# Optimization experiments

Hardware: AMD Instinct MI355X
Metric: run time of the kernel (lower is better)

## Reference

```python
import jax, jax.numpy as jnp
import numpy as np

B, H, W, C = 16, 64, 64, 192
NH, WS, SHIFT = 6, 8, 4          # heads, window size, shift (window//2)
DEPTH, MLP_R = 2, 4
N = WS * WS                      # tokens per window = 64
HD = C // NH                     # head dim = 32
SCALE = HD ** -0.5
TBL = (2 * WS - 1) ** 2          # relative-bias table size = 225
NW = (H // WS) * (W // WS)       # windows per image = 64


def _rel_pos_index():
    coords = np.stack(np.meshgrid(np.arange(WS), np.arange(WS), indexing='ij')).reshape(2, -1)
    rel = (coords[:, :, None] - coords[:, None, :]).transpose(1, 2, 0)
    rel[..., 0] += WS - 1
    rel[..., 1] += WS - 1
    rel[..., 0] *= 2 * WS - 1
    return jnp.asarray(rel.sum(-1))  # [N, N] int


def _attn_mask():
    # Swin shifted-window mask: region ids then pairwise -100 where ids differ.
    img = np.zeros((H, W))
    sl = (slice(0, -WS), slice(-WS, -SHIFT), slice(-SHIFT, None))
    cnt = 0
    for hs in sl:
        for ws in sl:
            img[hs, ws] = cnt
            cnt += 1
    mw = img.reshape(H // WS, WS, W // WS, WS).transpose(0, 2, 1, 3).reshape(-1, N)
    diff = mw[:, None, :] - mw[:, :, None]
    return jnp.asarray(np.where(diff != 0, -100.0, 0.0).astype(np.float32))  # [NW, N, N]


REL_IDX = _rel_pos_index()
ATTN_MASK = _attn_mask()


def _ln(x, g, b, eps=1e-5):
    mu = x.mean(-1, keepdims=True)
    var = ((x - mu) ** 2).mean(-1, keepdims=True)
    return (x - mu) * jax.lax.rsqrt(var + eps) * g + b


def setup_inputs() -> dict:
    key = jax.random.key(0)
    ks = jax.random.split(key, 8)
    s = 0.02
    return {
        'x': jax.random.normal(ks[0], (B, H * W, C), jnp.float32),
        'norm1_g': jnp.ones((DEPTH, C)), 'norm1_b': jnp.zeros((DEPTH, C)),
        'qkv_w': jax.random.normal(ks[1], (DEPTH, 3 * C, C)) * s,
        'qkv_b': jnp.zeros((DEPTH, 3 * C)),
        'bias_table': jax.random.normal(ks[2], (DEPTH, TBL, NH)) * s,
        'proj_w': jax.random.normal(ks[3], (DEPTH, C, C)) * s,
        'proj_b': jnp.zeros((DEPTH, C)),
        'norm2_g': jnp.ones((DEPTH, C)), 'norm2_b': jnp.zeros((DEPTH, C)),
        'fc1_w': jax.random.normal(ks[4], (DEPTH, MLP_R * C, C)) * s,
        'fc1_b': jnp.zeros((DEPTH, MLP_R * C)),
        'fc2_w': jax.random.normal(ks[5], (DEPTH, C, MLP_R * C)) * s,
        'fc2_b': jnp.zeros((DEPTH, C)),
    }


def _block(x, shift, n1g, n1b, qw, qb, tbl, pw, pb, n2g, n2b, f1w, f1b, f2w, f2b):
    shortcut = x
    y = _ln(x, n1g, n1b).reshape(B, H, W, C)
    if shift > 0:
        y = jnp.roll(y, (-shift, -shift), axis=(1, 2))
    # window partition -> [B*NW, N, C]
    win = y.reshape(B, H // WS, WS, W // WS, WS, C).transpose(0, 1, 3, 2, 4, 5).reshape(-1, N, C)
    qkv = (win @ qw.T + qb).reshape(-1, N, 3, NH, HD).transpose(2, 0, 3, 1, 4)
    q, k, v = qkv[0] * SCALE, qkv[1], qkv[2]          # each [B*NW, NH, N, HD]
    attn = jnp.einsum('bhnd,bhmd->bhnm', q, k)
    attn = attn + tbl[REL_IDX].transpose(2, 0, 1)[None]  # relative position bias
    if shift > 0:
        attn = (attn.reshape(B, NW, NH, N, N) + ATTN_MASK[None, :, None]).reshape(-1, NH, N, N)
    attn = jax.nn.softmax(attn, axis=-1)
    o = jnp.einsum('bhnm,bhmd->bhnd', attn, v).transpose(0, 2, 1, 3).reshape(-1, N, C)
    o = o @ pw.T + pb
    # window reverse
    y = o.reshape(B, H // WS, W // WS, WS, WS, C).transpose(0, 1, 3, 2, 4, 5).reshape(B, H, W, C)
    if shift > 0:
        y = jnp.roll(y, (shift, shift), axis=(1, 2))
    x = shortcut + y.reshape(B, H * W, C)
    h = _ln(x, n2g, n2b)
    h = jax.nn.gelu(h @ f1w.T + f1b, approximate=False)  # torch nn.GELU = exact erf
    return x + (h @ f2w.T + f2b)


def reference(x, norm1_g, norm1_b, qkv_w, qkv_b, bias_table, proj_w, proj_b,
              norm2_g, norm2_b, fc1_w, fc1_b, fc2_w, fc2_b):
    for i in range(DEPTH):
        shift = 0 if i % 2 == 0 else SHIFT
        x = _block(x, shift, norm1_g[i], norm1_b[i], qkv_w[i], qkv_b[i], bias_table[i],
                   proj_w[i], proj_b[i], norm2_g[i], norm2_b[i],
                   fc1_w[i], fc1_b[i], fc2_w[i], fc2_b[i])
    return x
```

## Files before the change

### kernel.cpp

```cpp
#include <hip/hip_runtime.h>
#include <hip/hip_bf16.h>
#include <math.h>

typedef __hip_bfloat16 bf16;
typedef short bf16x8 __attribute__((ext_vector_type(8)));
typedef short s16x4 __attribute__((ext_vector_type(4)));
typedef float f32x4 __attribute__((ext_vector_type(4)));

#define TOKENS 65536
#define C_ 192

__device__ __forceinline__ float b2f(bf16 v){ return __bfloat162float(v); }
__device__ __forceinline__ bf16 f2b(float v){ return __float2bfloat16(v); }
__device__ __forceinline__ short f2s(float v){
  bf16 b = __float2bfloat16(v);
  union { bf16 b; short s; } u; u.b = b; return u.s;
}
__device__ __forceinline__ float s2f(short s){
  union { unsigned u; float f; } c; c.u = ((unsigned)(unsigned short)s) << 16; return c.f;
}

__global__ void detect_k(const unsigned* __restrict__ g, int* __restrict__ flag){
  *flag = (g[0] == 0x3F800000u) ? 1 : 0;
}
__global__ void xconv_k(const void* __restrict__ x, float* __restrict__ y, int n,
                        const int* __restrict__ flag){
  int i = blockIdx.x*blockDim.x + threadIdx.x;
  if (i >= n) return;
  if (*flag) y[i] = ((const float*)x)[i];
  else       y[i] = b2f(((const bf16*)x)[i]);
}
struct WPtrs { const void* p[13]; };
__global__ void wconv_all_k(WPtrs wp, const int* __restrict__ offs, const int* __restrict__ lens,
                            bf16* __restrict__ dst, int total, const int* __restrict__ flag){
  int i = blockIdx.x*blockDim.x + threadIdx.x;
  if (i >= total) return;
  int t = 0;
  while (t < 12 && i >= offs[t+1]) t++;
  int j = i - offs[t];
  if (j >= lens[t]) return;
  if (*flag) dst[i] = f2b(((const float*)wp.p[t])[j]);
  else       dst[i] = ((const bf16*)wp.p[t])[j];
}
__global__ void outconv_k(const float* __restrict__ x, void* __restrict__ y, int n,
                          const int* __restrict__ flag){
  int i = blockIdx.x*blockDim.x + threadIdx.x;
  if (i >= n) return;
  if (*flag) ((float*)y)[i] = x[i];
  else       ((bf16*)y)[i]  = f2b(x[i]);
}

__global__ void bias_setup_k(const bf16* __restrict__ bt, float* __restrict__ biasF){
  int idx = blockIdx.x*blockDim.x + threadIdx.x;
  if (idx >= 2*6*64*64) return;
  int v = idx & 63;
  int lane = (idx >> 6) & 63;
  int rest = idx >> 12;
  int head = rest % 6, dd = rest / 6;
  int jt = v >> 4, it = (v >> 2) & 3, r = v & 3;
  int quad = lane >> 4, lr = lane & 15;
  int j = jt*16 + quad*4 + r;
  int i = it*16 + lr;
  int rel = ((i>>3) - (j>>3) + 7)*15 + ((i&7) - (j&7) + 7);
  biasF[idx] = b2f(bt[(dd*225 + rel)*6 + head]);
}

__global__ void mlp_repack_k(const bf16* __restrict__ f1w, const bf16* __restrict__ f2w,
                             bf16* __restrict__ w1p, bf16* __restrict__ w2p){
  int id = blockIdx.x*blockDim.x + threadIdx.x;
  if (id >= 589824) return;
  int arr = id / 294912;
  int r = id % 294912;
  int d = r / 147456;
  int e = r % 147456;
  int j = e & 7, lane = (e >> 3) & 63, frag = e >> 9;
  int lr = lane & 15, quad = lane >> 4;
  if (arr == 0){
    int ks = frag % 6, t = frag / 6;
    int mh = t & 1, cc = t >> 1;
    w1p[(size_t)d*147456 + e] =
        f1w[(size_t)d*147456 + (size_t)(cc*32 + mh*16 + lr)*192 + ks*32 + quad*8 + j];
  } else {
    int ct = frag % 12, cc = frag / 12;
    w2p[(size_t)d*147456 + e] =
        f2w[(size_t)d*147456 + (size_t)(ct*16 + lr)*768 + cc*32 + quad*8 + j];
  }
}

__global__ __launch_bounds__(768, 1) void attn_fused_k(float* __restrict__ xres,
    const bf16* __restrict__ n1g, const bf16* __restrict__ n1b,
    const bf16* __restrict__ qw, const bf16* __restrict__ qb,
    const bf16* __restrict__ pw, const bf16* __restrict__ pb,
    const float* __restrict__ biasF, int shift)
{
  extern __shared__ char smem[];
  short* xo = (short*)smem;
  int win = blockIdx.x;
  int tid = threadIdx.x;
  int wave = tid >> 6, lane = tid & 63;
  int quad = lane >> 4, lr = lane & 15;
  int head = wave >> 1, half = wave & 1;
  int b_ = win >> 6, wl = win & 63, wh = wl >> 3, wwi = wl & 7;
  short* kh  = (short*)(smem + 25600 + head*17408);
  short* vth = kh + 2048;
  short* qP  = vth + 2304;

  int c0 = lane*3;
  float g0 = b2f(n1g[c0]), g1 = b2f(n1g[c0+1]), g2 = b2f(n1g[c0+2]);
  float e0 = b2f(n1b[c0]), e1 = b2f(n1b[c0+1]), e2 = b2f(n1b[c0+2]);
  #pragma unroll
  for (int p = 0; p < 6; p++){
    int tok = p*12 + wave;
    if (tok < 64){
      int hh = (wh*8 + (tok>>3) + shift) & 63, ww = (wwi*8 + (tok&7) + shift) & 63;
      const float* rowp = xres + ((size_t)(b_<<12) + (hh<<6) + ww)*C_;
      float v0 = rowp[c0], v1 = rowp[c0+1], v2 = rowp[c0+2];
      float s = v0+v1+v2;
      #pragma unroll
      for (int off=32; off; off>>=1) s += __shfl_xor(s, off);
      float mu = s * (1.0f/192.0f);
      float d0=v0-mu, d1=v1-mu, d2=v2-mu;
      float q = d0*d0+d1*d1+d2*d2;
      #pragma unroll
      for (int off=32; off; off>>=1) q += __shfl_xor(q, off);
      float rstd = rsqrtf(q*(1.0f/192.0f) + 1e-5f);
      xo[tok*200 + c0]   = f2s(d0*rstd*g0 + e0);
      xo[tok*200 + c0+1] = f2s(d1*rstd*g1 + e1);
      xo[tok*200 + c0+2] = f2s(d2*rstd*g2 + e2);
    }
  }
  __syncthreads();

  const short* qwd = (const short*)qw;
  #pragma unroll
  for (int cc = 0; cc < 3; cc++){
    int nbase = cc*192 + head*32;
    f32x4 acc[2][2];
    #pragma unroll
    for (int mt = 0; mt < 2; mt++)
      #pragma unroll
      for (int nt = 0; nt < 2; nt++) acc[mt][nt] = (f32x4){0.f,0.f,0.f,0.f};
    #pragma unroll
    for (int ks = 0; ks < 6; ks++){
      bf16x8 af[2], bx[2];
      #pragma unroll
      for (int mt = 0; mt < 2; mt++)
        af[mt] = *(const bf16x8*)(qwd + (size_t)(nbase + mt*16 + lr)*192 + ks*32 + quad*8);
      #pragma unroll
      for (int nt = 0; nt < 2; nt++)
        bx[nt] = *(const bf16x8*)&xo[((2*half + nt)*16 + lr)*200 + ks*32 + quad*8];
      #pragma unroll
      for (int mt = 0; mt < 2; mt++)
        #pragma unroll
        for (int nt = 0; nt < 2; nt++)
          acc[mt][nt] = __builtin_amdgcn_mfma_f32_16x16x32_bf16(af[mt], bx[nt], acc[mt][nt], 0, 0, 0);
    }
    #pragma unroll
    for (int mt = 0; mt < 2; mt++){
      float bv[4];
      #pragma unroll
      for (int r = 0; r < 4; r++) bv[r] = b2f(qb[nbase + mt*16 + quad*4 + r]);
      #pragma unroll
      for (int nt = 0; nt < 2; nt++){
        int tok = (2*half + nt)*16 + lr;
        if (cc == 0){
          s16x4 pk;
          #pragma unroll
          for (int r = 0; r < 4; r++) pk[r] = f2s((acc[mt][nt][r] + bv[r]) * 0.17677669529663689f);
          *(s16x4*)&qP[tok*32 + mt*16 + quad*4] = pk;
        } else if (cc == 1){
          s16x4 pk;
          #pragma unroll
          for (int r = 0; r < 4; r++) pk[r] = f2s(acc[mt][nt][r] + bv[r]);
          *(s16x4*)&kh[tok*32 + mt*16 + quad*4] = pk;
        } else {
          #pragma unroll
          for (int r = 0; r < 4; r++)
            vth[(mt*16 + quad*4 + r)*72 + tok] = f2s(acc[mt][nt][r] + bv[r]);
        }
      }
    }
  }
  __syncthreads();

  bf16x8 ak[4], bq[2];
  #pragma unroll
  for (int jt = 0; jt < 4; jt++) ak[jt] = *(const bf16x8*)&kh[(jt*16 + lr)*32 + quad*8];
  #pragma unroll
  for (int it = 0; it < 2; it++)
    bq[it] = *(const bf16x8*)&qP[((2*half + it)*16 + lr)*32 + quad*8];
  __syncthreads();

  f32x4 S[4][2];
  #pragma unroll
  for (int jt = 0; jt < 4; jt++)
    #pragma unroll
    for (int it = 0; it < 2; it++) S[jt][it] = (f32x4){0.f,0.f,0.f,0.f};
  #pragma unroll
  for (int jt = 0; jt < 4; jt++)
    #pragma unroll
    for (int it = 0; it < 2; it++)
      S[jt][it] = __builtin_amdgcn_mfma_f32_16x16x32_bf16(ak[jt], bq[it], S[jt][it], 0, 0, 0);

  const f32x4* bm = (const f32x4*)(biasF + ((size_t)head*64 + lane)*64);
  #pragma unroll
  for (int jt = 0; jt < 4; jt++)
    #pragma unroll
    for (int it = 0; it < 2; it++) S[jt][it] += bm[jt*4 + 2*half + it];

  if (shift){
    int idi[2];
    #pragma unroll
    for (int it = 0; it < 2; it++){
      int itg = 2*half + it;
      int hh = wh*8 + itg*2 + (lr >> 3);
      int wwc = wwi*8 + (lr & 7);
      idi[it] = (hh < 56 ? 0 : (hh < 60 ? 1 : 2))*3 + (wwc < 56 ? 0 : (wwc < 60 ? 1 : 2));
    }
    #pragma unroll
    for (int jt = 0; jt < 4; jt++)
      #pragma unroll
      for (int r = 0; r < 4; r++){
        int j = jt*16 + quad*4 + r;
        int hh = wh*8 + (j >> 3), wwc = wwi*8 + (j & 7);
        int idj = (hh < 56 ? 0 : (hh < 60 ? 1 : 2))*3 + (wwc < 56 ? 0 : (wwc < 60 ? 1 : 2));
        #pragma unroll
        for (int it = 0; it < 2; it++)
          if (idj != idi[it]) S[jt][it][r] -= 100.f;
      }
  }
  #pragma unroll
  for (int it = 0; it < 2; it++){
    float m = -1e30f;
    #pragma unroll
    for (int jt = 0; jt < 4; jt++)
      #pragma unroll
      for (int r = 0; r < 4; r++) m = fmaxf(m, S[jt][it][r]);
    m = fmaxf(m, __shfl_xor(m, 16));
    m = fmaxf(m, __shfl_xor(m, 32));
    float s = 0.f;
    #pragma unroll
    for (int jt = 0; jt < 4; jt++)
      #pragma unroll
      for (int r = 0; r < 4; r++){
        float e = __expf(S[jt][it][r] - m);
        S[jt][it][r] = e; s += e;
      }
    s += __shfl_xor(s, 16);
    s += __shfl_xor(s, 32);
    float inv = 1.0f / s;
    #pragma unroll
    for (int jt = 0; jt < 4; jt++){
      s16x4 pk;
      #pragma unroll
      for (int r = 0; r < 4; r++) pk[r] = f2s(S[jt][it][r] * inv);
      *(s16x4*)&qP[((2*half + it)*16 + lr)*68 + jt*16 + quad*4] = pk;
    }
  }
  __syncthreads();

  bf16x8 va[2][2], pv[2][2];
  #pragma unroll
  for (int mt = 0; mt < 2; mt++)
    #pragma unroll
    for (int ks = 0; ks < 2; ks++)
      va[mt][ks] = *(const bf16x8*)&vth[(mt*16 + lr)*72 + ks*32 + quad*8];
  #pragma unroll
  for (int nt = 0; nt < 2; nt++)
    #pragma unroll
    for (int ks = 0; ks < 2; ks++)
      pv[nt][ks] = *(const bf16x8*)&qP[((2*half + nt)*16 + lr)*68 + ks*32 + quad*8];

  f32x4 O[2][2];
  #pragma unroll
  for (int mt = 0; mt < 2; mt++)
    #pragma unroll
    for (int nt = 0; nt < 2; nt++) O[mt][nt] = (f32x4){0.f,0.f,0.f,0.f};
  #pragma unroll
  for (int mt = 0; mt < 2; mt++)
    #pragma unroll
    for (int nt = 0; nt < 2; nt++)
      #pragma unroll
      for (int ks = 0; ks < 2; ks++)
        O[mt][nt] = __builtin_amdgcn_mfma_f32_16x16x32_bf16(va[mt][ks], pv[nt][ks], O[mt][nt], 0, 0, 0);

  #pragma unroll
  for (int mt = 0; mt < 2; mt++)
    #pragma unroll
    for (int nt = 0; nt < 2; nt++){
      s16x4 pk;
      #pragma unroll
      for (int r = 0; r < 4; r++) pk[r] = f2s(O[mt][nt][r]);
      *(s16x4*)&xo[((2*half + nt)*16 + lr)*200 + head*32 + mt*16 + quad*4] = pk;
    }
  __syncthreads();

  int wm = wave / 6, wn = wave % 6;
  f32x4 po[2][2];
  #pragma unroll
  for (int mt = 0; mt < 2; mt++)
    #pragma unroll
    for (int nt = 0; nt < 2; nt++) po[mt][nt] = (f32x4){0.f,0.f,0.f,0.f};
  const short* pwd = (const short*)pw;
  #pragma unroll
  for (int ks = 0; ks < 6; ks++){
    bf16x8 ao[2], bw[2];
    #pragma unroll
    for (int mt = 0; mt < 2; mt++)
      ao[mt] = *(const bf16x8*)&xo[(wm*32 + mt*16 + lr)*200 + ks*32 + quad*8];
    #pragma unroll
    for (int nt = 0; nt < 2; nt++)
      bw[nt] = *(const bf16x8*)(pwd + (size_t)(wn*32 + nt*16 + lr)*192 + ks*32 + quad*8);
    #pragma unroll
    for (int mt = 0; mt < 2; mt++)
      #pragma unroll
      for (int nt = 0; nt < 2; nt++)
        po[mt][nt] = __builtin_amdgcn_mfma_f32_16x16x32_bf16(ao[mt], bw[nt], po[mt][nt], 0, 0, 0);
  }
  #pragma unroll
  for (int nt = 0; nt < 2; nt++){
    int n = wn*32 + nt*16 + lr;
    float bv = b2f(pb[n]);
    #pragma unroll
    for (int mt = 0; mt < 2; mt++){
      #pragma unroll
      for (int r = 0; r < 4; r++){
        int tok = wm*32 + mt*16 + quad*4 + r;
        int hh = (wh*8 + (tok>>3) + shift) & 63, ww = (wwi*8 + (tok&7) + shift) & 63;
        float* dst = xres + ((size_t)(b_<<12) + (hh<<6) + ww)*C_ + n;
        *dst += po[mt][nt][r] + bv;
      }
    }
  }
}

__global__ __launch_bounds__(512, 4) void mlp_coop_k(float* __restrict__ xres,
    const bf16* __restrict__ n2g, const bf16* __restrict__ n2b,
    const bf16* __restrict__ w1p, const bf16* __restrict__ f1b,
    const bf16* __restrict__ w2p, const bf16* __restrict__ f2bv)
{
  __shared__ short Wst[2][24*512];
  __shared__ short HsAll[8][16*36];
  int tid = threadIdx.x;
  int wave = tid >> 6, lane = tid & 63;
  int quad = lane >> 4, lr = lane & 15;
  short* Hs = HsAll[wave];
  int t0 = blockIdx.x*128 + wave*16;

  const short* w1 = (const short*)w1p;
  const short* w2 = (const short*)w2p;

  int f0 = wave*3;

  bf16x8 rg[3];
  #pragma unroll
  for (int k = 0; k < 3; k++){
    int f = f0 + k;
    const short* g = (f < 12) ? (w1 + (size_t)f*512 + lane*8)
                              : (w2 + (size_t)(f - 12)*512 + lane*8);
    rg[k] = *(const bf16x8*)g;
  }

  bf16x8 xh[6];
  {
    const float* rowp = xres + (size_t)(t0 + lr)*C_;
    float v[6][8];
    float s = 0.f;
    #pragma unroll
    for (int ks = 0; ks < 6; ks++){
      int cb = ks*32 + quad*8;
      #pragma unroll
      for (int j = 0; j < 8; j++){ v[ks][j] = rowp[cb+j]; s += v[ks][j]; }
    }
    s += __shfl_xor(s, 16); s += __shfl_xor(s, 32);
    float mu = s*(1.0f/192.0f);
    float q = 0.f;
    #pragma unroll
    for (int ks = 0; ks < 6; ks++)
      #pragma unroll
      for (int j = 0; j < 8; j++){ float d = v[ks][j]-mu; q += d*d; }
    q += __shfl_xor(q, 16); q += __shfl_xor(q, 32);
    float rstd = rsqrtf(q*(1.0f/192.0f) + 1e-5f);
    #pragma unroll
    for (int ks = 0; ks < 6; ks++){
      int cb = ks*32 + quad*8;
      #pragma unroll
      for (int j = 0; j < 8; j++)
        xh[ks][j] = f2s((v[ks][j]-mu)*rstd*b2f(n2g[cb+j]) + b2f(n2b[cb+j]));
    }
  }

  #pragma unroll
  for (int k = 0; k < 3; k++)
    *(bf16x8*)&Wst[0][(f0 + k)*512 + lane*8] = rg[k];

  f32x4 acc[12];
  #pragma unroll
  for (int ct = 0; ct < 12; ct++) acc[ct] = (f32x4){0.f,0.f,0.f,0.f};

  int cur = 0;
  for (int cc = 0; cc < 24; cc++){
    if (cc < 23){
      #pragma unroll
      for (int k = 0; k < 3; k++){
        int f = f0 + k;
        const short* g = (f < 12) ? (w1 + (size_t)((cc+1)*12 + f)*512 + lane*8)
                                  : (w2 + (size_t)((cc+1)*12 + (f - 12))*512 + lane*8);
        rg[k] = *(const bf16x8*)g;
      }
    }

    __syncthreads();

    const short* rdb = &Wst[cur][0];

    f32x4 hacc[2];
    hacc[0] = (f32x4){0.f,0.f,0.f,0.f};
    hacc[1] = (f32x4){0.f,0.f,0.f,0.f};
    #pragma unroll
    for (int ks = 0; ks < 6; ks++){
      bf16x8 af0 = *(const bf16x8*)&rdb[ks*512 + lane*8];
      bf16x8 af1 = *(const bf16x8*)&rdb[(6 + ks)*512 + lane*8];
      hacc[0] = __builtin_amdgcn_mfma_f32_16x16x32_bf16(af0, xh[ks], hacc[0], 0, 0, 0);
      hacc[1] = __builtin_amdgcn_mfma_f32_16x16x32_bf16(af1, xh[ks], hacc[1], 0, 0, 0);
    }
    #pragma unroll
    for (int mh = 0; mh < 2; mh++){
      s16x4 bb = *(const s16x4*)((const short*)f1b + cc*32 + mh*16 + quad*4);
      s16x4 pk;
      #pragma unroll
      for (int r = 0; r < 4; r++){
        float x = hacc[mh][r] + s2f(bb[r]);
        float y = x*(0.7978845608f + 0.0356774081f*x*x);
        float t = __expf(2.0f*fminf(y, 9.0f));
        pk[r] = f2s(x*t/(t + 1.0f));
      }
      *(s16x4*)&Hs[lr*36 + mh*16 + quad*4] = pk;
    }
    bf16x8 ah = *(const bf16x8*)&Hs[lr*36 + quad*8];
    #pragma unroll
    for (int ct = 0; ct < 12; ct++){
      bf16x8 bw = *(const bf16x8*)&rdb[(12 + ct)*512 + lane*8];
      acc[ct] = __builtin_amdgcn_mfma_f32_16x16x32_bf16(bw, ah, acc[ct], 0, 0, 0);
    }

    if (cc < 23){
      #pragma unroll
      for (int k = 0; k < 3; k++)
        *(bf16x8*)&Wst[cur ^ 1][(f0 + k)*512 + lane*8] = rg[k];
    }
    cur ^= 1;
  }

  {
    int m = t0 + lr;
    float* rowd = xres + (size_t)m*C_;
    #pragma unroll
    for (int ct = 0; ct < 12; ct++){
      int n0 = ct*16 + quad*4;
      s16x4 bb = *(const s16x4*)((const short*)f2bv + n0);
      f32x4* dst = (f32x4*)(rowd + n0);
      f32x4 cur4 = *dst;
      #pragma unroll
      for (int r = 0; r < 4; r++) cur4[r] += acc[ct][r] + s2f(bb[r]);
      *dst = cur4;
    }
  }
}

extern "C" void kernel_launch(void* const* d_in, const int* in_sizes, int n_in,
                              void* d_out, int out_size, void* d_ws, size_t ws_size,
                              hipStream_t stream)
{
  (void)in_sizes; (void)n_in; (void)out_size;

  if (ws_size < (size_t)52117000) return;
  char* ws = (char*)d_ws;
  float* xf   = (float*)ws;
  bf16* canon = (bf16*)(ws + 50331648);
  int*  flagp = (int*)(ws + 52116608);
  float* biasF = (float*)d_out;
  bf16* w1p = (bf16*)((char*)d_out + 196608);
  bf16* w2p = (bf16*)((char*)d_out + 786432);

  static const int W_OFF[13] = {0, 384, 768, 221952, 223104, 225856, 299584,
                                299968, 300352, 300736, 595648, 597184, 892096};
  const int W_TOTAL = 892480;

  hipFuncSetAttribute((const void*)attn_fused_k,
                      hipFuncAttributeMaxDynamicSharedMemorySize, 130048);

  detect_k<<<1, 1, 0, stream>>>((const unsigned*)d_in[1], flagp);

  WPtrs wp;
  for (int i = 0; i < 13; i++) wp.p[i] = d_in[i+1];
  {
    int* meta = (int*)(ws + 52116672);
    struct Init {
      static __global__ void run(int* meta){
        const int offs[13] = {0, 384, 768, 221952, 223104, 225856, 299584,
                              299968, 300352, 300736, 595648, 597184, 892096};
        const int lens[13] = {384, 384, 221184, 1152, 2700, 73728, 384,
                              384, 384, 294912, 1536, 294912, 384};
        int i = threadIdx.x;
        if (i < 13){ meta[i] = offs[i]; meta[13+i] = lens[i]; }
      }
    };
    hipLaunchKernelGGL(Init::run, dim3(1), dim3(16), 0, stream, meta);
    wconv_all_k<<<(W_TOTAL + 255)/256, 256, 0, stream>>>(wp, meta, meta+13, canon, W_TOTAL, flagp);
  }

  const int nelem = TOKENS*C_;
  xconv_k<<<nelem/256, 256, 0, stream>>>(d_in[0], xf, nelem, flagp);

  const bf16* n1g = canon + W_OFF[0];
  const bf16* n1b = canon + W_OFF[1];
  const bf16* qw  = canon + W_OFF[2];
  const bf16* qb  = canon + W_OFF[3];
  const bf16* bt  = canon + W_OFF[4];
  const bf16* pw  = canon + W_OFF[5];
  const bf16* pb  = canon + W_OFF[6];
  const bf16* n2g = canon + W_OFF[7];
  const bf16* n2b = canon + W_OFF[8];
  const bf16* f1w = canon + W_OFF[9];
  const bf16* f1b = canon + W_OFF[10];
  const bf16* f2w = canon + W_OFF[11];
  const bf16* f2bv= canon + W_OFF[12];

  bias_setup_k<<<(2*6*64*64)/256, 256, 0, stream>>>(bt, biasF);
  mlp_repack_k<<<(589824 + 255)/256, 256, 0, stream>>>(f1w, f2w, w1p, w2p);

  for (int d = 0; d < 2; d++){
    int shift = d ? 4 : 0;
    attn_fused_k<<<1024, 768, 130048, stream>>>(xf,
        n1g + d*192, n1b + d*192, qw + d*576*192, qb + d*576,
        pw + d*192*192, pb + d*192, biasF + d*6*64*64, shift);
    mlp_coop_k<<<512, 512, 0, stream>>>(xf,
        n2g + d*192, n2b + d*192, w1p + d*147456, f1b + d*768,
        w2p + d*147456, f2bv + d*192);
  }
  outconv_k<<<nelem/256, 256, 0, stream>>>(xf, d_out, nelem, flagp);
}
```

Before: 581.1 us.

## Merge setup kernels and pad K/Q shared-memory rows to avoid bank conflicts

Folds dtype detection, weight conversion, input conversion, bias setup and MLP repack into two combined kernels, removing several small launches and the flag round trip through memory. It also pads the per-head K and Q rows in LDS from 32 to 40 bf16 elements, aiming to cut bank conflicts on the 16-byte fragment loads. Dynamic shared memory grows from 130048 to 136192 bytes. Each thread now reads the first weight word to re-derive the dtype flag.

```diff
diff --git a/kernel.cpp b/kernel.cpp
--- a/kernel.cpp
+++ b/kernel.cpp
@@ -20,54 +20,60 @@
   union { unsigned u; float f; } c; c.u = ((unsigned)(unsigned short)s) << 16; return c.f;
 }
 
-__global__ void detect_k(const unsigned* __restrict__ g, int* __restrict__ flag){
-  *flag = (g[0] == 0x3F800000u) ? 1 : 0;
-}
-__global__ void xconv_k(const void* __restrict__ x, float* __restrict__ y, int n,
-                        const int* __restrict__ flag){
+struct WPtrs { const void* p[13]; };
+#define W_TOTAL_ 892480
+#define NELEM_ (TOKENS*C_)
+__global__ void convert_k(WPtrs wp, const void* __restrict__ x,
+                          bf16* __restrict__ canon, float* __restrict__ xf){
+  const int offs[13] = {0, 384, 768, 221952, 223104, 225856, 299584,
+                        299968, 300352, 300736, 595648, 597184, 892096};
+  const int lens[13] = {384, 384, 221184, 1152, 2700, 73728, 384,
+                        384, 384, 294912, 1536, 294912, 384};
+  int flag = (*(const unsigned*)wp.p[0] == 0x3F800000u) ? 1 : 0;
+  int i = blockIdx.x*blockDim.x + threadIdx.x;
+  if (i < W_TOTAL_){
+    int t = 0;
+    while (t < 12 && i >= offs[t+1]) t++;
+    int j = i - offs[t];
+    if (j < lens[t]){
+      if (flag) canon[i] = f2b(((const float*)wp.p[t])[j]);
+      else      canon[i] = ((const bf16*)wp.p[t])[j];
+    }
+  } else {
+    int j = i - W_TOTAL_;
+    if (j < NELEM_){
+      if (flag) xf[j] = ((const float*)x)[j];
+      else      xf[j] = b2f(((const bf16*)x)[j]);
+    }
+  }
+}
+__global__ void outconv_k(const float* __restrict__ x, void* __restrict__ y, int n,
+                          const unsigned* __restrict__ g){
+  int flag = (g[0] == 0x3F800000u) ? 1 : 0;
   int i = blockIdx.x*blockDim.x + threadIdx.x;
   if (i >= n) return;
-  if (*flag) y[i] = ((const float*)x)[i];
-  else       y[i] = b2f(((const bf16*)x)[i]);
-}
-struct WPtrs { const void* p[13]; };
-__global__ void wconv_all_k(WPtrs wp, const int* __restrict__ offs, const int* __restrict__ lens,
-                            bf16* __restrict__ dst, int total, const int* __restrict__ flag){
-  int i = blockIdx.x*blockDim.x + threadIdx.x;
-  if (i >= total) return;
-  int t = 0;
-  while (t < 12 && i >= offs[t+1]) t++;
-  int j = i - offs[t];
-  if (j >= lens[t]) return;
-  if (*flag) dst[i] = f2b(((const float*)wp.p[t])[j]);
-  else       dst[i] = ((const bf16*)wp.p[t])[j];
-}
-__global__ void outconv_k(const float* __restrict__ x, void* __restrict__ y, int n,
-                          const int* __restrict__ flag){
-  int i = blockIdx.x*blockDim.x + threadIdx.x;
-  if (i >= n) return;
-  if (*flag) ((float*)y)[i] = x[i];
-  else       ((bf16*)y)[i]  = f2b(x[i]);
-}
-
-__global__ void bias_setup_k(const bf16* __restrict__ bt, float* __restrict__ biasF){
+  if (flag) ((float*)y)[i] = x[i];
+  else      ((bf16*)y)[i]  = f2b(x[i]);
+}
+
+__global__ void setup_k(const bf16* __restrict__ bt, float* __restrict__ biasF,
+                        const bf16* __restrict__ f1w, const bf16* __restrict__ f2w,
+                        bf16* __restrict__ w1p, bf16* __restrict__ w2p){
   int idx = blockIdx.x*blockDim.x + threadIdx.x;
-  if (idx >= 2*6*64*64) return;
-  int v = idx & 63;
-  int lane = (idx >> 6) & 63;
-  int rest = idx >> 12;
-  int head = rest % 6, dd = rest / 6;
-  int jt = v >> 4, it = (v >> 2) & 3, r = v & 3;
-  int quad = lane >> 4, lr = lane & 15;
-  int j = jt*16 + quad*4 + r;
-  int i = it*16 + lr;
-  int rel = ((i>>3) - (j>>3) + 7)*15 + ((i&7) - (j&7) + 7);
-  biasF[idx] = b2f(bt[(dd*225 + rel)*6 + head]);
-}
-
-__global__ void mlp_repack_k(const bf16* __restrict__ f1w, const bf16* __restrict__ f2w,
-                             bf16* __restrict__ w1p, bf16* __restrict__ w2p){
-  int id = blockIdx.x*blockDim.x + threadIdx.x;
+  if (idx < 2*6*64*64){
+    int v = idx & 63;
+    int lane = (idx >> 6) & 63;
+    int rest = idx >> 12;
+    int head = rest % 6, dd = rest / 6;
+    int jt = v >> 4, it = (v >> 2) & 3, r = v & 3;
+    int quad = lane >> 4, lr = lane & 15;
+    int j = jt*16 + quad*4 + r;
+    int i = it*16 + lr;
+    int rel = ((i>>3) - (j>>3) + 7)*15 + ((i&7) - (j&7) + 7);
+    biasF[idx] = b2f(bt[(dd*225 + rel)*6 + head]);
+    return;
+  }
+  int id = idx - 2*6*64*64;
   if (id >= 589824) return;
   int arr = id / 294912;
   int r = id % 294912;
@@ -101,8 +107,8 @@
   int quad = lane >> 4, lr = lane & 15;
   int head = wave >> 1, half = wave & 1;
   int b_ = win >> 6, wl = win & 63, wh = wl >> 3, wwi = wl & 7;
-  short* kh  = (short*)(smem + 25600 + head*17408);
-  short* vth = kh + 2048;
+  short* kh  = (short*)(smem + 25600 + head*18432);
+  short* vth = kh + 2560;
   short* qP  = vth + 2304;
 
   int c0 = lane*3;
@@ -167,12 +173,12 @@
           s16x4 pk;
           #pragma unroll
           for (int r = 0; r < 4; r++) pk[r] = f2s((acc[mt][nt][r] + bv[r]) * 0.17677669529663689f);
-          *(s16x4*)&qP[tok*32 + mt*16 + quad*4] = pk;
+          *(s16x4*)&qP[tok*40 + mt*16 + quad*4] = pk;
         } else if (cc == 1){
           s16x4 pk;
           #pragma unroll
           for (int r = 0; r < 4; r++) pk[r] = f2s(acc[mt][nt][r] + bv[r]);
-          *(s16x4*)&kh[tok*32 + mt*16 + quad*4] = pk;
+          *(s16x4*)&kh[tok*40 + mt*16 + quad*4] = pk;
         } else {
           #pragma unroll
           for (int r = 0; r < 4; r++)
@@ -185,10 +191,10 @@
 
   bf16x8 ak[4], bq[2];
   #pragma unroll
-  for (int jt = 0; jt < 4; jt++) ak[jt] = *(const bf16x8*)&kh[(jt*16 + lr)*32 + quad*8];
+  for (int jt = 0; jt < 4; jt++) ak[jt] = *(const bf16x8*)&kh[(jt*16 + lr)*40 + quad*8];
   #pragma unroll
   for (int it = 0; it < 2; it++)
-    bq[it] = *(const bf16x8*)&qP[((2*half + it)*16 + lr)*32 + quad*8];
+    bq[it] = *(const bf16x8*)&qP[((2*half + it)*16 + lr)*40 + quad*8];
   __syncthreads();
 
   f32x4 S[4][2];
@@ -478,40 +484,21 @@
   char* ws = (char*)d_ws;
   float* xf   = (float*)ws;
   bf16* canon = (bf16*)(ws + 50331648);
-  int*  flagp = (int*)(ws + 52116608);
   float* biasF = (float*)d_out;
   bf16* w1p = (bf16*)((char*)d_out + 196608);
   bf16* w2p = (bf16*)((char*)d_out + 786432);
 
   static const int W_OFF[13] = {0, 384, 768, 221952, 223104, 225856, 299584,
                                 299968, 300352, 300736, 595648, 597184, 892096};
-  const int W_TOTAL = 892480;
 
   hipFuncSetAttribute((const void*)attn_fused_k,
-                      hipFuncAttributeMaxDynamicSharedMemorySize, 130048);
-
-  detect_k<<<1, 1, 0, stream>>>((const unsigned*)d_in[1], flagp);
+                      hipFuncAttributeMaxDynamicSharedMemorySize, 136192);
 
   WPtrs wp;
   for (int i = 0; i < 13; i++) wp.p[i] = d_in[i+1];
-  {
-    int* meta = (int*)(ws + 52116672);
-    struct Init {
-      static __global__ void run(int* meta){
-        const int offs[13] = {0, 384, 768, 221952, 223104, 225856, 299584,
-                              299968, 300352, 300736, 595648, 597184, 892096};
-        const int lens[13] = {384, 384, 221184, 1152, 2700, 73728, 384,
-                              384, 384, 294912, 1536, 294912, 384};
-        int i = threadIdx.x;
-        if (i < 13){ meta[i] = offs[i]; meta[13+i] = lens[i]; }
-      }
-    };
-    hipLaunchKernelGGL(Init::run, dim3(1), dim3(16), 0, stream, meta);
-    wconv_all_k<<<(W_TOTAL + 255)/256, 256, 0, stream>>>(wp, meta, meta+13, canon, W_TOTAL, flagp);
-  }
 
   const int nelem = TOKENS*C_;
-  xconv_k<<<nelem/256, 256, 0, stream>>>(d_in[0], xf, nelem, flagp);
+  convert_k<<<(W_TOTAL_ + nelem + 255)/256, 256, 0, stream>>>(wp, d_in[0], canon, xf);
 
   const bf16* n1g = canon + W_OFF[0];
   const bf16* n1b = canon + W_OFF[1];
@@ -527,17 +514,16 @@
   const bf16* f2w = canon + W_OFF[11];
   const bf16* f2bv= canon + W_OFF[12];
 
-  bias_setup_k<<<(2*6*64*64)/256, 256, 0, stream>>>(bt, biasF);
-  mlp_repack_k<<<(589824 + 255)/256, 256, 0, stream>>>(f1w, f2w, w1p, w2p);
+  setup_k<<<(49152 + 589824 + 255)/256, 256, 0, stream>>>(bt, biasF, f1w, f2w, w1p, w2p);
 
   for (int d = 0; d < 2; d++){
     int shift = d ? 4 : 0;
-    attn_fused_k<<<1024, 768, 130048, stream>>>(xf,
+    attn_fused_k<<<1024, 768, 136192, stream>>>(xf,
         n1g + d*192, n1b + d*192, qw + d*576*192, qb + d*576,
         pw + d*192*192, pb + d*192, biasF + d*6*64*64, shift);
     mlp_coop_k<<<512, 512, 0, stream>>>(xf,
         n2g + d*192, n2b + d*192, w1p + d*147456, f1b + d*768,
         w2p + d*147456, f2bv + d*192);
   }
-  outconv_k<<<nelem/256, 256, 0, stream>>>(xf, d_out, nelem, flagp);
-}
+  outconv_k<<<nelem/256, 256, 0, stream>>>(xf, d_out, nelem, (const unsigned*)d_in[1]);
+}
```

New measurement: 575.7 us. About the same (-0.9%).
